# Optimization experiments

Measured on AMD Instinct MI355X. Metric: run time of the kernel, lower is better.

The kernel has to match this reference:

```python
import jax, jax.numpy as jnp
import numpy as np

TAU = 100.0
DT = 20.0
ALPHA = DT / TAU  # 0.2, fixed buffer (train_alpha=False)


def setup_inputs() -> dict:
    key = jax.random.key(0)
    ks = jax.random.split(key, 12)
    T, B, I, H = 64, 32, 128, 256

    def lin(kw, out_f, in_f):
        bound = 1.0 / np.sqrt(in_f)
        kw1, kw2 = jax.random.split(kw)
        w = jax.random.uniform(kw1, (out_f, in_f), jnp.float32, -bound, bound)
        b = jax.random.uniform(kw2, (out_f,), jnp.float32, -bound, bound)
        return w, b

    w_i2h, b_i2h = lin(ks[0], H, I)
    w_h2h, b_h2h = lin(ks[1], H, H)
    w_i2c, b_i2c = lin(ks[2], H, I)
    w_c2c, b_c2c = lin(ks[3], H, H)
    w_c2t, b_c2t = lin(ks[4], H * H, H)
    x = jax.random.normal(ks[5], (T, B, I), jnp.float32)
    return {
        "input": x,
        "w_i2h": w_i2h, "b_i2h": b_i2h,
        "w_h2h": w_h2h, "b_h2h": b_h2h,
        "w_i2c": w_i2c, "b_i2c": b_i2c,
        "w_c2c": w_c2c, "b_c2c": b_c2c,
        "w_c2t": w_c2t, "b_c2t": b_c2t,
        "num_steps": 1,
    }


def reference(input, w_i2h, b_i2h, w_h2h, b_h2h, w_i2c, b_i2c,
              w_c2c, b_c2c, w_c2t, b_c2t, num_steps):
    H = w_i2h.shape[0]
    B = input.shape[1]
    a = jnp.float32(ALPHA)

    def recurrence(x, hidden, context):
        input_proj = x @ w_i2h.T + b_i2h                      # [B,H]
        tm = (context @ w_c2t.T + b_c2t).reshape(B, H, H)     # per-sample hypernet matrix
        transformed = jnp.einsum('bij,bj->bi', tm, input_proj)
        h_new = jax.nn.relu(context + transformed + hidden @ w_h2h.T + b_h2h)
        hidden = hidden * (1 - a) + h_new * a
        context_new = jax.nn.relu(context @ w_c2c.T + b_c2c + x @ w_i2c.T + b_i2c)
        context = context * (1 - a) + context_new * a
        hidden = transformed  # NOTE: faithful to source, overwrites leaky update
        return hidden, context

    def step(carry, x):
        hidden, context = carry
        for _ in range(num_steps):
            hidden, context = recurrence(x, hidden, context)
        return (hidden, context), hidden

    h0 = jnp.zeros((B, H), input.dtype)
    c0 = jnp.zeros((B, H), input.dtype)
    (hidden, context), output = jax.lax.scan(step, (h0, c0), input)
    return output, hidden, context
```

## Files before the change

### kernel.cpp

```cpp
#include <hip/hip_runtime.h>

#define TT 64
#define BB 32
#define II 128
#define HH 256
#define MM (TT*BB)

typedef __bf16  bf16x8  __attribute__((ext_vector_type(8)));
typedef float   f32x16  __attribute__((ext_vector_type(16)));
typedef _Float16 half2v __attribute__((ext_vector_type(2)));

__device__ __forceinline__ float bf2f(unsigned short u) {
    union { unsigned int i; float f; } v; v.i = ((unsigned int)u) << 16; return v.f;
}
__device__ __forceinline__ unsigned short f2bf(float f) {
    union { float f; unsigned int i; } v; v.f = f;
    unsigned int r = v.i + 0x7fffu + ((v.i >> 16) & 1u);
    return (unsigned short)(r >> 16);
}

struct F8 { float v[8]; };
__device__ __forceinline__ F8 load8(const void* base, int idx, int isf32) {
    F8 r;
    if (isf32) {
        const float4* p = (const float4*)((const float*)base + idx);
        float4 a = p[0], b = p[1];
        r.v[0]=a.x; r.v[1]=a.y; r.v[2]=a.z; r.v[3]=a.w;
        r.v[4]=b.x; r.v[5]=b.y; r.v[6]=b.z; r.v[7]=b.w;
    } else {
        uint4 u = *(const uint4*)((const unsigned short*)base + idx);
        const unsigned short* p = (const unsigned short*)&u;
#pragma unroll
        for (int j = 0; j < 8; ++j) r.v[j] = bf2f(p[j]);
    }
    return r;
}
__device__ __forceinline__ float load1(const void* base, int idx, int isf32) {
    return isf32 ? ((const float*)base)[idx]
                 : bf2f(((const unsigned short*)base)[idx]);
}

__device__ __forceinline__ float fdot2f(half2v a, half2v b, float c) {
#if __has_builtin(__builtin_amdgcn_fdot2)
    return __builtin_amdgcn_fdot2(a, b, c, false);
#else
    return c + (float)a.x*(float)b.x + (float)a.y*(float)b.y;
#endif
}

__global__ __launch_bounds__(256) void k0_sniff(
    const unsigned short* __restrict__ x, int* __restrict__ flag)
{
    __shared__ int cnt;
    if (threadIdx.x == 0) cnt = 0;
    __syncthreads();
    int c = 0;
    for (int i = threadIdx.x; i < 8192; i += 256) {
        unsigned int e = (x[i] >> 7) & 0xFFu;
        if (e >= 0xC0u) ++c;
    }
    atomicAdd(&cnt, c);
    __syncthreads();
    if (threadIdx.x == 0) flag[0] = (cnt > 16) ? 1 : 0;
}

__global__ __launch_bounds__(256) void k1_proj(
    const void* __restrict__ x,
    const void* __restrict__ w_i2h,
    const void* __restrict__ b_i2h,
    const void* __restrict__ w_i2c,
    const void* __restrict__ b_i2c,
    const int* __restrict__ flagp,
    unsigned short* __restrict__ ip,
    float* __restrict__ cin)
{
    const int isf32 = *flagp;
    const int tid = threadIdx.x;
    const int h = tid;
    const int mbase = blockIdx.x * 32;
    __shared__ __align__(16) _Float16 xs[32][II];

    half2v w1[II/2], w2[II/2];
#pragma unroll
    for (int c8 = 0; c8 < II/8; ++c8) {
        F8 f1 = load8(w_i2h, h*II + c8*8, isf32);
        F8 f2 = load8(w_i2c, h*II + c8*8, isf32);
#pragma unroll
        for (int j = 0; j < 4; ++j) {
            half2v a; a.x = (_Float16)f1.v[2*j]; a.y = (_Float16)f1.v[2*j+1];
            half2v b; b.x = (_Float16)f2.v[2*j]; b.y = (_Float16)f2.v[2*j+1];
            w1[c8*4 + j] = a;
            w2[c8*4 + j] = b;
        }
    }
    const float bb1 = load1(b_i2h, h, isf32);
    const float bb2 = load1(b_i2c, h, isf32);

    for (int u = tid; u < 32*II; u += 256)
        xs[u >> 7][u & (II-1)] = (_Float16)load1(x, (mbase + (u >> 7))*II + (u & (II-1)), isf32);
    __syncthreads();

    for (int mm = 0; mm < 32; ++mm) {
        const half2v* xv = (const half2v*)xs[mm];
        float a0=0,a1=0,a2=0,a3=0, c0=0,c1=0,c2=0,c3=0;
#pragma unroll
        for (int r = 0; r < II/2; r += 4) {
            half2v x0 = xv[r], x1 = xv[r+1], x2 = xv[r+2], x3 = xv[r+3];
            a0 = fdot2f(w1[r],   x0, a0);
            a1 = fdot2f(w1[r+1], x1, a1);
            a2 = fdot2f(w1[r+2], x2, a2);
            a3 = fdot2f(w1[r+3], x3, a3);
            c0 = fdot2f(w2[r],   x0, c0);
            c1 = fdot2f(w2[r+1], x1, c1);
            c2 = fdot2f(w2[r+2], x2, c2);
            c3 = fdot2f(w2[r+3], x3, c3);
        }
        ip[(mbase+mm)*HH + h]  = f2bf(((a0+a1)+(a2+a3)) + bb1);
        cin[(mbase+mm)*HH + h] = ((c0+c1)+(c2+c3)) + bb2;
    }
}

__global__ __launch_bounds__(256) void k2_ctx(
    const void* __restrict__ w_c2c,
    const void* __restrict__ b_c2c,
    const float* __restrict__ cin,
    const int* __restrict__ ns_ptr,
    const int* __restrict__ flagp,
    unsigned short* __restrict__ ctx_hist,
    void* __restrict__ out_base)
{
    const int isf32 = *flagp;
    const int b = blockIdx.x;
    const int h = threadIdx.x;
    const int ns = max(1, *ns_ptr);

    __shared__ __align__(16) _Float16 cs[2][HH];

    half2v w[HH/2];
#pragma unroll
    for (int c8 = 0; c8 < HH/8; ++c8) {
        F8 f = load8(w_c2c, h*HH + c8*8, isf32);
#pragma unroll
        for (int j = 0; j < 4; ++j) {
            half2v hv;
            hv.x = (_Float16)f.v[2*j];
            hv.y = (_Float16)f.v[2*j+1];
            w[c8*4 + j] = hv;
        }
    }
    const float bcc = load1(b_c2c, h, isf32);
    float ctxv = 0.0f;
    cs[0][h] = (_Float16)0.0f;
    __syncthreads();
    int cur = 0;

    for (int t = 0; t < TT; ++t) {
        const float cinv = cin[(t*BB + b)*HH + h];
        for (int s = 0; s < ns; ++s) {
            if (s == ns-1) ctx_hist[(t*BB + b)*HH + h] = f2bf(ctxv);
            float p0=0,p1=0,p2=0,p3=0;
            const float4* cp4 = (const float4*)cs[cur];
#pragma unroll
            for (int r4 = 0; r4 < HH/8; ++r4) {
                float4 blob = cp4[r4];
                const half2v* c2 = (const half2v*)&blob;
                p0 = fdot2f(w[r4*4+0], c2[0], p0);
                p1 = fdot2f(w[r4*4+1], c2[1], p1);
                p2 = fdot2f(w[r4*4+2], c2[2], p2);
                p3 = fdot2f(w[r4*4+3], c2[3], p3);
            }
            float cnew = fmaxf(((p0+p1)+(p2+p3)) + bcc + cinv, 0.0f);
            ctxv = 0.8f*ctxv + 0.2f*cnew;
            cs[cur^1][h] = (_Float16)ctxv;
            cur ^= 1;
            __syncthreads();
        }
    }
    const int cofs = MM*HH + BB*HH + b*HH + h;
    if (isf32) ((float*)out_base)[cofs] = ctxv;
    else       ((unsigned short*)out_base)[cofs] = f2bf(ctxv);
}

__global__ __launch_bounds__(512, 2) void k3_main(
    const unsigned short* __restrict__ ctx_hist,
    const void* __restrict__ wc,
    const void* __restrict__ bc,
    const unsigned short* __restrict__ ip,
    const int* __restrict__ flagp,
    void* __restrict__ out)
{
    extern __shared__ __align__(16) unsigned char lds[];
    unsigned short* Ws = (unsigned short*)lds;
    unsigned short* As = (unsigned short*)(lds + 131072);
    float*          Ps = (float*)(lds + 131072);

    const int isf32 = *flagp;
    const int tid  = threadIdx.x;
    const int lane = tid & 63;
    const int wave = tid >> 6;
    const int i    = blockIdx.x;
    const int jq   = wave & 3;
    const int mh   = wave >> 1 >> 1;
    const int l31  = lane & 31;
    const int lhi  = lane >> 5;

    float bcv[2][4][4];
#pragma unroll
    for (int a = 0; a < 2; ++a)
#pragma unroll
        for (int g = 0; g < 4; ++g) {
            const int j0 = i*HH + jq*64 + a*32 + lhi*4 + g*8;
            if (isf32) {
                float4 t = *(const float4*)((const float*)bc + j0);
                bcv[a][g][0]=t.x; bcv[a][g][1]=t.y; bcv[a][g][2]=t.z; bcv[a][g][3]=t.w;
            } else {
                ushort4 t = *(const ushort4*)((const unsigned short*)bc + j0);
                bcv[a][g][0]=bf2f(t.x); bcv[a][g][1]=bf2f(t.y);
                bcv[a][g][2]=bf2f(t.z); bcv[a][g][3]=bf2f(t.w);
            }
        }

#pragma unroll
    for (int p = 0; p < 16; ++p) {
        int u = tid + p*512;
        int row = u >> 5, cu = u & 31;
        F8 f = load8(wc, (i*HH + row)*HH + cu*8, isf32);
        unsigned short tmp[8];
#pragma unroll
        for (int j = 0; j < 8; ++j) tmp[j] = f2bf(f.v[j]);
        *(uint4*)(Ws + row*256 + ((cu ^ (row & 7)) << 3)) = *(const uint4*)tmp;
    }

    uint4 gbuf[4];
#pragma unroll
    for (int p = 0; p < 4; ++p) {
        const int u = tid + p*512;
        gbuf[p] = *(const uint4*)(ctx_hist + (u >> 3)*HH + (u & 7)*8);
    }

    for (int mc = 0; mc < 8; ++mc) {
        const int m0 = mc * 256;

        f32x16 acc[2][4];
#pragma unroll
        for (int a = 0; a < 2; ++a)
#pragma unroll
            for (int n = 0; n < 4; ++n)
#pragma unroll
                for (int r = 0; r < 16; ++r) acc[a][n][r] = 0.0f;

#pragma unroll
        for (int kc = 0; kc < 4; ++kc) {
            __syncthreads();
#pragma unroll
            for (int p = 0; p < 4; ++p) {
                const int u = tid + p*512;
                const int row = u >> 3, cu = u & 7;
                *(uint4*)(As + row*64 + ((cu ^ (row & 7)) << 3)) = gbuf[p];
            }
            {
                const int nc  = (mc*4 + kc + 1) & 31;
                const int nm0 = (nc >> 2) * 256, nk0 = (nc & 3) * 64;
#pragma unroll
                for (int p = 0; p < 4; ++p) {
                    const int u = tid + p*512;
                    gbuf[p] = *(const uint4*)(ctx_hist + (nm0 + (u >> 3))*HH + nk0 + (u & 7)*8);
                }
            }
            __syncthreads();
#pragma unroll
            for (int ks = 0; ks < 4; ++ks) {
                const int cB  = kc*8 + ks*2 + lhi;
                const int rj0 = jq*64 + l31;
                const int rj1 = rj0 + 32;
                bf16x8 w0 = *(const bf16x8*)(Ws + rj0*256 + ((cB ^ (rj0 & 7)) << 3));
                bf16x8 w1 = *(const bf16x8*)(Ws + rj1*256 + ((cB ^ (rj1 & 7)) << 3));
                const int cA  = ks*2 + lhi;
                const int rm0 = mh*128 +      l31;
                const int rm1 = rm0 + 32;
                const int rm2 = rm0 + 64;
                const int rm3 = rm0 + 96;
                bf16x8 c0 = *(const bf16x8*)(As + rm0*64 + ((cA ^ (rm0 & 7)) << 3));
                bf16x8 c1 = *(const bf16x8*)(As + rm1*64 + ((cA ^ (rm1 & 7)) << 3));
                bf16x8 c2 = *(const bf16x8*)(As + rm2*64 + ((cA ^ (rm2 & 7)) << 3));
                bf16x8 c3 = *(const bf16x8*)(As + rm3*64 + ((cA ^ (rm3 & 7)) << 3));
                acc[0][0] = __builtin_amdgcn_mfma_f32_32x32x16_bf16(w0, c0, acc[0][0], 0, 0, 0);
                acc[0][1] = __builtin_amdgcn_mfma_f32_32x32x16_bf16(w0, c1, acc[0][1], 0, 0, 0);
                acc[0][2] = __builtin_amdgcn_mfma_f32_32x32x16_bf16(w0, c2, acc[0][2], 0, 0, 0);
                acc[0][3] = __builtin_amdgcn_mfma_f32_32x32x16_bf16(w0, c3, acc[0][3], 0, 0, 0);
                acc[1][0] = __builtin_amdgcn_mfma_f32_32x32x16_bf16(w1, c0, acc[1][0], 0, 0, 0);
                acc[1][1] = __builtin_amdgcn_mfma_f32_32x32x16_bf16(w1, c1, acc[1][1], 0, 0, 0);
                acc[1][2] = __builtin_amdgcn_mfma_f32_32x32x16_bf16(w1, c2, acc[1][2], 0, 0, 0);
                acc[1][3] = __builtin_amdgcn_mfma_f32_32x32x16_bf16(w1, c3, acc[1][3], 0, 0, 0);
            }
        }

        float sv[4];
#pragma unroll
        for (int n = 0; n < 4; ++n) {
            const unsigned short* iprow =
                ip + (m0 + mh*128 + n*32 + l31)*HH + jq*64 + lhi*4;
            float s = 0.0f;
#pragma unroll
            for (int a = 0; a < 2; ++a)
#pragma unroll
                for (int g = 0; g < 4; ++g) {
                    ushort4 t = *(const ushort4*)(iprow + a*32 + g*8);
                    s = fmaf(acc[a][n][g*4+0] + bcv[a][g][0], bf2f(t.x), s);
                    s = fmaf(acc[a][n][g*4+1] + bcv[a][g][1], bf2f(t.y), s);
                    s = fmaf(acc[a][n][g*4+2] + bcv[a][g][2], bf2f(t.z), s);
                    s = fmaf(acc[a][n][g*4+3] + bcv[a][g][3], bf2f(t.w), s);
                }
            s += __shfl_xor(s, 32);
            sv[n] = s;
        }
        __syncthreads();
        if (lhi == 0) {
#pragma unroll
            for (int n = 0; n < 4; ++n)
                Ps[jq*256 + mh*128 + n*32 + l31] = sv[n];
        }
        __syncthreads();
        if (tid < 256) {
            const float r = Ps[tid] + Ps[256+tid] + Ps[512+tid] + Ps[768+tid];
            const int gr = m0 + tid;
            if (isf32) {
                float* o = (float*)out;
                o[gr*HH + i] = r;
                if (gr >= MM - BB) o[MM*HH + (gr - (MM-BB))*HH + i] = r;
            } else {
                unsigned short* o = (unsigned short*)out;
                const unsigned short v = f2bf(r);
                o[gr*HH + i] = v;
                if (gr >= MM - BB) o[MM*HH + (gr - (MM-BB))*HH + i] = v;
            }
        }
    }
}

extern "C" void kernel_launch(void* const* d_in, const int* in_sizes, int n_in,
                              void* d_out, int out_size, void* d_ws, size_t ws_size,
                              hipStream_t stream) {
    const void* x     = d_in[0];
    const void* w_i2h = d_in[1];
    const void* b_i2h = d_in[2];
    const void* w_i2c = d_in[5];
    const void* b_i2c = d_in[6];
    const void* w_c2c = d_in[7];
    const void* b_c2c = d_in[8];
    const void* w_c2t = d_in[9];
    const void* b_c2t = d_in[10];
    const int* ns     = (const int*)d_in[11];

    unsigned short* ip  = (unsigned short*)d_ws;
    unsigned short* ch  = (unsigned short*)((char*)d_ws + (size_t)MM*HH*2);
    float* cin          = (float*)((char*)d_ws + (size_t)MM*HH*4);
    int* flag           = (int*)((char*)d_ws + (size_t)MM*HH*8);

    (void)hipFuncSetAttribute((const void*)k3_main,
                              hipFuncAttributeMaxDynamicSharedMemorySize, 163840);

    k0_sniff<<<1, 256, 0, stream>>>((const unsigned short*)x, flag);
    k1_proj<<<64, 256, 0, stream>>>(x, w_i2h, b_i2h, w_i2c, b_i2c, flag, ip, cin);
    k2_ctx<<<BB, 256, 0, stream>>>(w_c2c, b_c2c, cin, ns, flag, ch, d_out);
    k3_main<<<256, 512, 163840, stream>>>(ch, w_c2t, b_c2t, ip, flag, d_out);
}
```

Baseline: 370.9 us.

## Transpose input-projection and output buffers for coalesced access in main kernel

```diff
diff --git a/kernel.cpp b/kernel.cpp
--- a/kernel.cpp
+++ b/kernel.cpp
@@ -71,7 +71,7 @@
     const void* __restrict__ w_i2c,
     const void* __restrict__ b_i2c,
     const int* __restrict__ flagp,
-    unsigned short* __restrict__ ip,
+    unsigned short* __restrict__ ipT,
     float* __restrict__ cin)
 {
     const int isf32 = *flagp;
@@ -79,6 +79,7 @@
     const int h = tid;
     const int mbase = blockIdx.x * 32;
     __shared__ __align__(16) _Float16 xs[32][II];
+    __shared__ __align__(16) unsigned short ips[32][HH];
 
     half2v w1[II/2], w2[II/2];
 #pragma unroll
@@ -115,9 +116,16 @@
             c2 = fdot2f(w2[r+2], x2, c2);
             c3 = fdot2f(w2[r+3], x3, c3);
         }
-        ip[(mbase+mm)*HH + h]  = f2bf(((a0+a1)+(a2+a3)) + bb1);
+        ips[mm][h] = f2bf(((a0+a1)+(a2+a3)) + bb1);
         cin[(mbase+mm)*HH + h] = ((c0+c1)+(c2+c3)) + bb2;
     }
+    __syncthreads();
+    unsigned short tmp[32];
+#pragma unroll
+    for (int mm = 0; mm < 32; ++mm) tmp[mm] = ips[mm][tid];
+    uint4* dst = (uint4*)(ipT + (size_t)tid*MM + mbase);
+    const uint4* s4 = (const uint4*)tmp;
+    dst[0] = s4[0]; dst[1] = s4[1]; dst[2] = s4[2]; dst[3] = s4[3];
 }
 
 __global__ __launch_bounds__(256) void k2_ctx(
@@ -185,9 +193,9 @@
     const unsigned short* __restrict__ ctx_hist,
     const void* __restrict__ wc,
     const void* __restrict__ bc,
-    const unsigned short* __restrict__ ip,
+    const unsigned short* __restrict__ ipT,
     const int* __restrict__ flagp,
-    void* __restrict__ out)
+    float* __restrict__ outT)
 {
     extern __shared__ __align__(16) unsigned char lds[];
     unsigned short* Ws = (unsigned short*)lds;
@@ -200,7 +208,7 @@
     const int wave = tid >> 6;
     const int i    = blockIdx.x;
     const int jq   = wave & 3;
-    const int mh   = wave >> 1 >> 1;
+    const int mh   = wave >> 2;
     const int l31  = lane & 31;
     const int lhi  = lane >> 5;
 
@@ -258,6 +266,7 @@
                 const int row = u >> 3, cu = u & 7;
                 *(uint4*)(As + row*64 + ((cu ^ (row & 7)) << 3)) = gbuf[p];
             }
+            __syncthreads();
             {
                 const int nc  = (mc*4 + kc + 1) & 31;
                 const int nm0 = (nc >> 2) * 256, nk0 = (nc & 3) * 64;
@@ -267,7 +276,6 @@
                     gbuf[p] = *(const uint4*)(ctx_hist + (nm0 + (u >> 3))*HH + nk0 + (u & 7)*8);
                 }
             }
-            __syncthreads();
 #pragma unroll
             for (int ks = 0; ks < 4; ++ks) {
                 const int cB  = kc*8 + ks*2 + lhi;
@@ -298,18 +306,18 @@
         float sv[4];
 #pragma unroll
         for (int n = 0; n < 4; ++n) {
-            const unsigned short* iprow =
-                ip + (m0 + mh*128 + n*32 + l31)*HH + jq*64 + lhi*4;
+            const unsigned short* ipcol = ipT + (size_t)(m0 + mh*128 + n*32 + l31);
             float s = 0.0f;
 #pragma unroll
             for (int a = 0; a < 2; ++a)
 #pragma unroll
                 for (int g = 0; g < 4; ++g) {
-                    ushort4 t = *(const ushort4*)(iprow + a*32 + g*8);
-                    s = fmaf(acc[a][n][g*4+0] + bcv[a][g][0], bf2f(t.x), s);
-                    s = fmaf(acc[a][n][g*4+1] + bcv[a][g][1], bf2f(t.y), s);
-                    s = fmaf(acc[a][n][g*4+2] + bcv[a][g][2], bf2f(t.z), s);
-                    s = fmaf(acc[a][n][g*4+3] + bcv[a][g][3], bf2f(t.w), s);
+                    const int jb = jq*64 + a*32 + lhi*4 + g*8;
+#pragma unroll
+                    for (int q = 0; q < 4; ++q) {
+                        const float ipv = bf2f(ipcol[(size_t)(jb + q)*MM]);
+                        s = fmaf(acc[a][n][g*4+q] + bcv[a][g][q], ipv, s);
+                    }
                 }
             s += __shfl_xor(s, 32);
             sv[n] = s;
@@ -323,17 +331,43 @@
         __syncthreads();
         if (tid < 256) {
             const float r = Ps[tid] + Ps[256+tid] + Ps[512+tid] + Ps[768+tid];
-            const int gr = m0 + tid;
-            if (isf32) {
-                float* o = (float*)out;
-                o[gr*HH + i] = r;
-                if (gr >= MM - BB) o[MM*HH + (gr - (MM-BB))*HH + i] = r;
-            } else {
-                unsigned short* o = (unsigned short*)out;
-                const unsigned short v = f2bf(r);
-                o[gr*HH + i] = v;
-                if (gr >= MM - BB) o[MM*HH + (gr - (MM-BB))*HH + i] = v;
-            }
+            outT[(size_t)i*MM + m0 + tid] = r;
+        }
+    }
+}
+
+__global__ __launch_bounds__(256) void k4_tr(
+    const float* __restrict__ outT,
+    const int* __restrict__ flagp,
+    void* __restrict__ out)
+{
+    const int isf32 = *flagp;
+    __shared__ float tile[64][65];
+    const int t  = threadIdx.x;
+    const int bm = blockIdx.x * 64;
+    const int bi = blockIdx.y * 64;
+#pragma unroll
+    for (int p = 0; p < 16; ++p) {
+        const int u = t + p*256;
+        const int r = u >> 6, c = u & 63;
+        tile[r][c] = outT[(size_t)(bi + r)*MM + bm + c];
+    }
+    __syncthreads();
+#pragma unroll
+    for (int p = 0; p < 16; ++p) {
+        const int u = t + p*256;
+        const int r = u >> 6, c = u & 63;
+        const float v = tile[c][r];
+        const int m = bm + r;
+        if (isf32) {
+            float* o = (float*)out;
+            o[(size_t)m*HH + bi + c] = v;
+            if (m >= MM - BB) o[(size_t)MM*HH + (m - (MM-BB))*HH + bi + c] = v;
+        } else {
+            unsigned short* o = (unsigned short*)out;
+            const unsigned short vb = f2bf(v);
+            o[(size_t)m*HH + bi + c] = vb;
+            if (m >= MM - BB) o[(size_t)MM*HH + (m - (MM-BB))*HH + bi + c] = vb;
         }
     }
 }
@@ -352,16 +386,18 @@
     const void* b_c2t = d_in[10];
     const int* ns     = (const int*)d_in[11];
 
-    unsigned short* ip  = (unsigned short*)d_ws;
+    unsigned short* ipT = (unsigned short*)d_ws;
     unsigned short* ch  = (unsigned short*)((char*)d_ws + (size_t)MM*HH*2);
     float* cin          = (float*)((char*)d_ws + (size_t)MM*HH*4);
+    float* outT         = cin;
     int* flag           = (int*)((char*)d_ws + (size_t)MM*HH*8);
 
     (void)hipFuncSetAttribute((const void*)k3_main,
                               hipFuncAttributeMaxDynamicSharedMemorySize, 163840);
 
     k0_sniff<<<1, 256, 0, stream>>>((const unsigned short*)x, flag);
-    k1_proj<<<64, 256, 0, stream>>>(x, w_i2h, b_i2h, w_i2c, b_i2c, flag, ip, cin);
+    k1_proj<<<64, 256, 0, stream>>>(x, w_i2h, b_i2h, w_i2c, b_i2c, flag, ipT, cin);
     k2_ctx<<<BB, 256, 0, stream>>>(w_c2c, b_c2c, cin, ns, flag, ch, d_out);
-    k3_main<<<256, 512, 163840, stream>>>(ch, w_c2t, b_c2t, ip, flag, d_out);
-}
+    k3_main<<<256, 512, 163840, stream>>>(ch, w_c2t, b_c2t, ipT, flag, outT);
+    k4_tr<<<dim3(32, 4), 256, 0, stream>>>(outT, flag, d_out);
+}
```

New measurement: 473.7 us. 1.28x slower.
